# Performance work log

Measured on AMD Instinct MI355X. Metric: run time of the kernel, lower is better.

The kernel has to match this reference:

```python
import jax, jax.numpy as jnp
import numpy as np

IN_F = 128
OUT_F = 64
HEAD = 4
ALPHA = 0.1
N, S = 32, 1024
OH = OUT_F * HEAD


def setup_inputs() -> dict:
    key = jax.random.key(0)
    k_h, k_adj, k_W, k_a = jax.random.split(key, 4)
    h = jax.random.normal(k_h, (N, S, IN_F), dtype=jnp.float32)
    adj = jax.random.uniform(k_adj, (N, S, S), dtype=jnp.float32)
    # xavier_uniform with gain=1.414
    gain = 1.414
    lim_W = gain * np.sqrt(6.0 / (IN_F + OH))
    W = jax.random.uniform(k_W, (IN_F, OH), dtype=jnp.float32, minval=-lim_W, maxval=lim_W)
    lim_a = gain * np.sqrt(6.0 / (2 * OH + 1))
    a = jax.random.uniform(k_a, (2 * OH, 1), dtype=jnp.float32, minval=-lim_a, maxval=lim_a)
    return {"h": h, "adj": adj, "W": W, "a": a}


def reference(h, adj, W, a):
    # h: (N, S, F_in); adj unused in original forward
    Wh = jnp.einsum('nsf,fo->nso', h, W)  # (N, S, OH)
    a1 = a[:OH, 0]   # source half of concat weight
    a2 = a[OH:, 0]   # target half
    # concat([Wh_i, Wh_j]) @ a == Wh_i@a1 + Wh_j@a2  (avoids (N,S,S,2*OH) tensor)
    f = Wh @ a1  # (N, S)
    g = Wh @ a2  # (N, S)
    e = f[:, :, None] + g[:, None, :]          # (N, S, S)
    e = jnp.where(e > 0, e, ALPHA * e)          # LeakyReLU
    attention = jax.nn.softmax(e, axis=2)
    out = jnp.einsum('nij,njo->nio', attention, Wh)  # (N, S, OH)
    # split into HEAD chunks of OUT_F, stack, mean over heads
    out = out.reshape(N, S, HEAD, OUT_F).mean(axis=2)
    # ELU
    return jnp.where(out > 0, out, jnp.expm1(out))
```

## Files before the change

### kernel.cpp

```cpp
#include <hip/hip_runtime.h>
#include <math.h>

#define SQ    1024
#define INF   128
#define OUTF  64
#define OHH   256
#define TSTR  66
#define LOG2E 1.44269504088896f

using bf16x8 = __attribute__((ext_vector_type(8))) __bf16;
using f32x4  = __attribute__((ext_vector_type(4))) float;
using u16x8  = __attribute__((ext_vector_type(8))) unsigned short;

#if __has_builtin(__builtin_amdgcn_exp2f)
#define EXP2F(x) __builtin_amdgcn_exp2f(x)
#else
#define EXP2F(x) __expf((x) * 0.6931471805599453f)
#endif

__global__ __launch_bounds__(256) void kA(
    const float* __restrict__ h, const float* __restrict__ W,
    const float* __restrict__ a, float* __restrict__ whm,
    float* __restrict__ fo, float* __restrict__ go)
{
    __shared__ __bf16 wmfH[8192];
    __shared__ __bf16 wmfL[8192];
    __shared__ float  wfl[INF], wgl[INF];
    __shared__ float  al[2 * OHH];

    const int t    = threadIdx.x;
    const int lane = t & 63;
    const int w    = t >> 6;
    const int bx   = blockIdx.x;
    const int R0   = ((bx & 31) << 10) + ((bx >> 5) << 6);

    al[t]       = a[t];
    al[t + 256] = a[t + 256];

    for (int g = t; g < 2048; g += 256) {
        const int k  = g >> 4;
        const int n0 = (g & 15) << 2;
        const float* Wp = W + k * OHH + n0;
        float4 w0 = *(const float4*)Wp;
        float4 w1 = *(const float4*)(Wp + 64);
        float4 w2 = *(const float4*)(Wp + 128);
        float4 w3 = *(const float4*)(Wp + 192);
        float wm4[4] = {0.25f * (w0.x + w1.x + w2.x + w3.x),
                        0.25f * (w0.y + w1.y + w2.y + w3.y),
                        0.25f * (w0.z + w1.z + w2.z + w3.z),
                        0.25f * (w0.w + w1.w + w2.w + w3.w)};
        const int c = k >> 5, kq = (k >> 3) & 3, id8 = k & 7, T = n0 >> 4;
        const int lbase = kq * 16 + (n0 & 15);
        #pragma unroll
        for (int j = 0; j < 4; ++j) {
            float  v  = wm4[j];
            __bf16 hb = (__bf16)v;
            const int o = ((c * 4 + T) * 64 + lbase + j) * 8 + id8;
            wmfH[o] = hb;
            wmfL[o] = (__bf16)(v - (float)hb);
        }
    }
    __syncthreads();

    {
        const int row = t & 127;
        const float4* Wr = (const float4*)(W + row * OHH);
        const float4* av = (const float4*)(t < 128 ? al : al + OHH);
        float s = 0.f;
        for (int q = 0; q < OHH / 4; ++q) {
            float4 wv = Wr[q], x = av[q];
            s += wv.x * x.x + wv.y * x.y + wv.z * x.z + wv.w * x.w;
        }
        if (t < 128) wfl[row] = s * LOG2E;
        else         wgl[row] = s * LOG2E;
    }
    __syncthreads();

    const int m  = lane & 15;
    const int kq = lane >> 4;
    const float* hrow = h + (size_t)(R0 + w * 16 + m) * INF + kq * 8;

    f32x4 acc[4] = {};
    float sf = 0.f, sg = 0.f;

    #pragma unroll
    for (int c = 0; c < 4; ++c) {
        float4 v0 = *(const float4*)(hrow + c * 32);
        float4 v1 = *(const float4*)(hrow + c * 32 + 4);
        float hv[8] = {v0.x, v0.y, v0.z, v0.w, v1.x, v1.y, v1.z, v1.w};

        float4 wf0 = *(const float4*)(wfl + c * 32 + kq * 8);
        float4 wf1 = *(const float4*)(wfl + c * 32 + kq * 8 + 4);
        float4 wg0 = *(const float4*)(wgl + c * 32 + kq * 8);
        float4 wg1 = *(const float4*)(wgl + c * 32 + kq * 8 + 4);
        float wfv[8] = {wf0.x, wf0.y, wf0.z, wf0.w, wf1.x, wf1.y, wf1.z, wf1.w};
        float wgv[8] = {wg0.x, wg0.y, wg0.z, wg0.w, wg1.x, wg1.y, wg1.z, wg1.w};

        u16x8  ahu;
        bf16x8 alo;
        #pragma unroll
        for (int i = 0; i < 8; ++i) {
            float v = hv[i];
            sf = fmaf(v, wfv[i], sf);
            sg = fmaf(v, wgv[i], sg);
            unsigned u = __float_as_uint(v);
            ahu[i] = (unsigned short)(u >> 16);
            alo[i] = (__bf16)(v - __uint_as_float(u & 0xFFFF0000u));
        }
        bf16x8 ah = __builtin_bit_cast(bf16x8, ahu);

        #pragma unroll
        for (int T = 0; T < 4; ++T) {
            bf16x8 bh = *(const bf16x8*)&wmfH[((c * 4 + T) * 64 + lane) * 8];
            bf16x8 bl = *(const bf16x8*)&wmfL[((c * 4 + T) * 64 + lane) * 8];
            acc[T] = __builtin_amdgcn_mfma_f32_16x16x32_bf16(ah,  bh, acc[T], 0, 0, 0);
            acc[T] = __builtin_amdgcn_mfma_f32_16x16x32_bf16(alo, bh, acc[T], 0, 0, 0);
            acc[T] = __builtin_amdgcn_mfma_f32_16x16x32_bf16(ah,  bl, acc[T], 0, 0, 0);
        }
    }

    sf += __shfl_xor(sf, 16, 64); sf += __shfl_xor(sf, 32, 64);
    sg += __shfl_xor(sg, 16, 64); sg += __shfl_xor(sg, 32, 64);
    if (lane < 16) {
        fo[R0 + w * 16 + m] = sf;
        go[R0 + w * 16 + m] = sg;
    }

    #pragma unroll
    for (int T = 0; T < 4; ++T) {
        #pragma unroll
        for (int r = 0; r < 4; ++r) {
            whm[(size_t)(R0 + w * 16 + kq * 4 + r) * OUTF + T * 16 + m] = acc[T][r];
        }
    }
}

__global__ __launch_bounds__(256) void kR(
    const float* __restrict__ gi, float* __restrict__ gs_out,
    unsigned short* __restrict__ piG)
{
    __shared__ unsigned long long keys[1024];

    const int t  = threadIdx.x;
    const int n  = blockIdx.x & 31;
    const int qb = blockIdx.x >> 5;

    for (int i = t; i < 1024; i += 256) {
        unsigned u   = __float_as_uint(gi[n * SQ + i]);
        unsigned key = (u & 0x80000000u) ? ~u : (u | 0x80000000u);
        keys[i] = ((unsigned long long)key << 32) | (unsigned)i;
    }
    __syncthreads();

    const int el = t >> 2;
    const int qt = t & 3;
    const int e  = qb * 64 + el;
    const unsigned long long Ke = keys[e];

    int cnt = 0;
    #pragma unroll 16
    for (int s = 0; s < 256; ++s) {
        int idx = qt * 256 + ((s + qt * 4) & 255);
        cnt += (keys[idx] < Ke) ? 1 : 0;
    }
    cnt += __shfl_xor(cnt, 1, 64);
    cnt += __shfl_xor(cnt, 2, 64);

    if (qt == 0) {
        unsigned kk = (unsigned)(Ke >> 32);
        unsigned uu = (kk & 0x80000000u) ? (kk & 0x7fffffffu) : ~kk;
        gs_out[n * SQ + cnt] = __uint_as_float(uu);
        piG[n * SQ + cnt]    = (unsigned short)e;
    }
}

__global__ __launch_bounds__(256) void kTB3(
    const float* __restrict__ whm, const unsigned short* __restrict__ piG,
    const float* __restrict__ gs,
    float* __restrict__ sufA, float* __restrict__ preB)
{
    __shared__ float          wsel[1024];
    __shared__ unsigned short piL[1024];
    __shared__ float          tot[16][TSTR];

    const int t    = threadIdx.x;
    const int lane = t & 63;
    const int wid  = t >> 6;
    const int n    = blockIdx.x & 31;
    const int k    = blockIdx.x >> 5;
    const int dir  = k & 1;
    const int qu   = k >> 1;

    for (int i = t; i < 1024; i += 256) {
        float g = gs[n * SQ + i];
        wsel[i] = EXP2F(dir ? g : 0.1f * g);
        piL[i]  = piG[n * SQ + i];
    }
    __syncthreads();

    const float* wb = whm + (size_t)n * (SQ * OUTF);

    for (int cc = 0; cc < 4; ++cc) {
        const int c = wid * 4 + cc;
        float acc = 0.f, dacc = 0.f;
        for (int q0 = 0; q0 < 64; q0 += 16) {
            float vals[16], wvv[16];
            #pragma unroll
            for (int u = 0; u < 16; ++u) {
                int tt = c * 64 + q0 + u;
                wvv[u]  = wsel[tt];
                vals[u] = wb[(size_t)piL[tt] * OUTF + lane];
            }
            #pragma unroll
            for (int u = 0; u < 16; ++u) {
                acc  = fmaf(wvv[u], vals[u], acc);
                dacc += wvv[u];
            }
        }
        tot[c][lane] = acc;
        if (lane == 0) tot[c][64] = dacc;
    }
    __syncthreads();

    const int c = qu * 4 + wid;
    float base = 0.f, based = 0.f;
    if (dir == 0) {
        for (int cc2 = 0; cc2 < c; ++cc2) {
            base  += tot[cc2][lane];
            based += tot[cc2][64];
        }
        float* Gp = preB + ((size_t)n * 1025 + (size_t)c * 64) * TSTR;
        float acc = base, dacc = based;
        for (int q0 = 0; q0 < 64; q0 += 16) {
            float vals[16], wvv[16];
            #pragma unroll
            for (int u = 0; u < 16; ++u) {
                int tt = c * 64 + q0 + u;
                wvv[u]  = wsel[tt];
                vals[u] = wb[(size_t)piL[tt] * OUTF + lane];
            }
            #pragma unroll
            for (int u = 0; u < 16; ++u) {
                float* row = Gp + (size_t)(q0 + u) * TSTR;
                row[lane] = acc;
                if (lane == 0) row[64] = dacc;
                acc  = fmaf(wvv[u], vals[u], acc);
                dacc += wvv[u];
            }
        }
        if (c == 15) {
            float* row = preB + ((size_t)n * 1025 + 1024) * TSTR;
            row[lane] = acc;
            if (lane == 0) row[64] = dacc;
        }
    } else {
        for (int cc2 = c + 1; cc2 < 16; ++cc2) {
            base  += tot[cc2][lane];
            based += tot[cc2][64];
        }
        float* Gs = sufA + ((size_t)n * 1025 + (size_t)c * 64) * TSTR;
        float acc = base, dacc = based;
        for (int q0 = 48; q0 >= 0; q0 -= 16) {
            float vals[16], wvv[16];
            #pragma unroll
            for (int u = 0; u < 16; ++u) {
                int tt = c * 64 + q0 + u;
                wvv[u]  = wsel[tt];
                vals[u] = wb[(size_t)piL[tt] * OUTF + lane];
            }
            #pragma unroll
            for (int u = 15; u >= 0; --u) {
                acc  = fmaf(wvv[u], vals[u], acc);
                dacc += wvv[u];
                float* row = Gs + (size_t)(q0 + u) * TSTR;
                row[lane] = acc;
                if (lane == 0) row[64] = dacc;
            }
        }
        if (c == 15) {
            float* row = sufA + ((size_t)n * 1025 + 1024) * TSTR;
            row[lane] = 0.f;
            if (lane == 0) row[64] = 0.f;
        }
    }
}

__global__ __launch_bounds__(256) void kD(
    const float* __restrict__ fi, const float* __restrict__ gs,
    const float* __restrict__ sufA, const float* __restrict__ preB,
    float* __restrict__ out)
{
    __shared__ float gsL[1025];

    const int t    = threadIdx.x;
    const int lane = t & 63;
    const int wid  = t >> 6;
    const int n    = blockIdx.x & 31;
    const int i0   = (blockIdx.x >> 5) * 64;

    for (int q = t; q < 1024; q += 256) gsL[q] = gs[n * SQ + q];
    if (t == 0) gsL[1024] = 3.0e38f;
    __syncthreads();

    const float myf = fi[n * SQ + i0 + wid * 16 + (lane & 15)];
    const float v = -myf;
    int lo = 0, hi = 1024;
    #pragma unroll
    for (int it = 0; it < 10; ++it) {
        int mid = (lo + hi) >> 1;
        bool gt = gsL[mid] > v;
        hi = gt ? mid : hi;
        lo = gt ? lo : mid + 1;
    }

    const float* SA = sufA + (size_t)n * 1025 * TSTR;
    const float* PB = preB + (size_t)n * 1025 * TSTR;
    const size_t orow0 = (size_t)(n * SQ + i0 + wid * 16);

    #pragma unroll 4
    for (int s = 0; s < 16; ++s) {
        int   r  = __shfl(lo,  s, 64);
        float fv = __shfl(myf, s, 64);
        const float* sa = SA + (size_t)r * TSTR;
        const float* pb = PB + (size_t)r * TSTR;
        float sv = sa[lane], pv = pb[lane];
        float sd = sa[64],  pd = pb[64];
        float eP = EXP2F(fv);
        float eN = EXP2F(0.1f * fv);
        float num = eP * sv + eN * pv;
        float den = eP * sd + eN * pd;
        float o = num / den;
        o = o > 0.f ? o : expm1f(o);
        out[(orow0 + s) * OUTF + lane] = o;
    }
}

extern "C" void kernel_launch(void* const* d_in, const int* in_sizes, int n_in,
                              void* d_out, int out_size, void* d_ws, size_t ws_size,
                              hipStream_t stream) {
    const float* h = (const float*)d_in[0];
    const float* W = (const float*)d_in[2];
    const float* a = (const float*)d_in[3];

    char* ws = (char*)d_ws;
    const size_t MB = 1024 * 1024;
    const size_t KB = 1024;
    float*          whm  = (float*)(ws);
    float*          fb   = (float*)(ws + 8 * MB);
    float*          gb   = (float*)(ws + 8 * MB + 128 * KB);
    float*          gsO  = (float*)(ws + 8 * MB + 256 * KB);
    unsigned short* piG  = (unsigned short*)(ws + 8 * MB + 384 * KB);
    float*          sufA = (float*)(ws + 10 * MB);
    float*          preB = (float*)(ws + 19 * MB);
    float*          outp = (float*)d_out;

    hipLaunchKernelGGL(kA,   dim3(512), dim3(256), 0, stream, h, W, a, whm, fb, gb);
    hipLaunchKernelGGL(kR,   dim3(512), dim3(256), 0, stream, gb, gsO, piG);
    hipLaunchKernelGGL(kTB3, dim3(256), dim3(256), 0, stream, whm, piG, gsO, sufA, preB);
    hipLaunchKernelGGL(kD,   dim3(512), dim3(256), 0, stream, fb, gsO, sufA, preB, outp);
}
```

Before: 227.6 us.

## Split prefix-scan into 32-row chunks, double kTB3 grid, reuse gathered rows

The prefix/suffix scan kernel now splits each batch's 1024 sorted rows into 32 chunks of 32 instead of 16 chunks of 64, and launches twice as many blocks. Each wave keeps the gathered values and weights for its own chunk in registers during the chunk-total pass, so the second gather from global memory is skipped. The kD output loop is also fully unrolled. In exchange, every block still recomputes the totals for all chunks, so redundant gather work doubles across the larger grid, and the 64 kept registers per thread raise register pressure.

```diff
diff --git a/kernel.cpp b/kernel.cpp
--- a/kernel.cpp
+++ b/kernel.cpp
@@ -181,7 +181,7 @@
 {
     __shared__ float          wsel[1024];
     __shared__ unsigned short piL[1024];
-    __shared__ float          tot[16][TSTR];
+    __shared__ float          tot[32][TSTR];
 
     const int t    = threadIdx.x;
     const int lane = t & 63;
@@ -189,7 +189,7 @@
     const int n    = blockIdx.x & 31;
     const int k    = blockIdx.x >> 5;
     const int dir  = k & 1;
-    const int qu   = k >> 1;
+    const int grp  = k >> 1;
 
     for (int i = t; i < 1024; i += 256) {
         float g = gs[n * SQ + i];
@@ -200,14 +200,16 @@
 
     const float* wb = whm + (size_t)n * (SQ * OUTF);
 
-    for (int cc = 0; cc < 4; ++cc) {
-        const int c = wid * 4 + cc;
+    float keepV[32], keepW[32];
+    for (int s8 = 0; s8 < 8; ++s8) {
+        const int sc = s8 * 4 + wid;
         float acc = 0.f, dacc = 0.f;
-        for (int q0 = 0; q0 < 64; q0 += 16) {
+        #pragma unroll
+        for (int h16 = 0; h16 < 2; ++h16) {
             float vals[16], wvv[16];
             #pragma unroll
             for (int u = 0; u < 16; ++u) {
-                int tt = c * 64 + q0 + u;
+                int tt = sc * 32 + h16 * 16 + u;
                 wvv[u]  = wsel[tt];
                 vals[u] = wb[(size_t)piL[tt] * OUTF + lane];
             }
@@ -216,68 +218,57 @@
                 acc  = fmaf(wvv[u], vals[u], acc);
                 dacc += wvv[u];
             }
-        }
-        tot[c][lane] = acc;
-        if (lane == 0) tot[c][64] = dacc;
-    }
-    __syncthreads();
-
-    const int c = qu * 4 + wid;
+            if (s8 == grp) {
+                #pragma unroll
+                for (int u = 0; u < 16; ++u) {
+                    keepV[h16 * 16 + u] = vals[u];
+                    keepW[h16 * 16 + u] = wvv[u];
+                }
+            }
+        }
+        tot[sc][lane] = acc;
+        if (lane == 0) tot[sc][64] = dacc;
+    }
+    __syncthreads();
+
+    const int sc = grp * 4 + wid;
     float base = 0.f, based = 0.f;
     if (dir == 0) {
-        for (int cc2 = 0; cc2 < c; ++cc2) {
-            base  += tot[cc2][lane];
-            based += tot[cc2][64];
-        }
-        float* Gp = preB + ((size_t)n * 1025 + (size_t)c * 64) * TSTR;
+        for (int s = 0; s < sc; ++s) {
+            base  += tot[s][lane];
+            based += tot[s][64];
+        }
+        float* Gp = preB + ((size_t)n * 1025 + (size_t)sc * 32) * TSTR;
         float acc = base, dacc = based;
-        for (int q0 = 0; q0 < 64; q0 += 16) {
-            float vals[16], wvv[16];
-            #pragma unroll
-            for (int u = 0; u < 16; ++u) {
-                int tt = c * 64 + q0 + u;
-                wvv[u]  = wsel[tt];
-                vals[u] = wb[(size_t)piL[tt] * OUTF + lane];
-            }
-            #pragma unroll
-            for (int u = 0; u < 16; ++u) {
-                float* row = Gp + (size_t)(q0 + u) * TSTR;
-                row[lane] = acc;
-                if (lane == 0) row[64] = dacc;
-                acc  = fmaf(wvv[u], vals[u], acc);
-                dacc += wvv[u];
-            }
-        }
-        if (c == 15) {
+        #pragma unroll
+        for (int u = 0; u < 32; ++u) {
+            float* row = Gp + (size_t)u * TSTR;
+            row[lane] = acc;
+            if (lane == 0) row[64] = dacc;
+            acc  = fmaf(keepW[u], keepV[u], acc);
+            dacc += keepW[u];
+        }
+        if (sc == 31) {
             float* row = preB + ((size_t)n * 1025 + 1024) * TSTR;
             row[lane] = acc;
             if (lane == 0) row[64] = dacc;
         }
     } else {
-        for (int cc2 = c + 1; cc2 < 16; ++cc2) {
-            base  += tot[cc2][lane];
-            based += tot[cc2][64];
-        }
-        float* Gs = sufA + ((size_t)n * 1025 + (size_t)c * 64) * TSTR;
+        for (int s = sc + 1; s < 32; ++s) {
+            base  += tot[s][lane];
+            based += tot[s][64];
+        }
+        float* Gs = sufA + ((size_t)n * 1025 + (size_t)sc * 32) * TSTR;
         float acc = base, dacc = based;
-        for (int q0 = 48; q0 >= 0; q0 -= 16) {
-            float vals[16], wvv[16];
-            #pragma unroll
-            for (int u = 0; u < 16; ++u) {
-                int tt = c * 64 + q0 + u;
-                wvv[u]  = wsel[tt];
-                vals[u] = wb[(size_t)piL[tt] * OUTF + lane];
-            }
-            #pragma unroll
-            for (int u = 15; u >= 0; --u) {
-                acc  = fmaf(wvv[u], vals[u], acc);
-                dacc += wvv[u];
-                float* row = Gs + (size_t)(q0 + u) * TSTR;
-                row[lane] = acc;
-                if (lane == 0) row[64] = dacc;
-            }
-        }
-        if (c == 15) {
+        #pragma unroll
+        for (int u = 31; u >= 0; --u) {
+            acc  = fmaf(keepW[u], keepV[u], acc);
+            dacc += keepW[u];
+            float* row = Gs + (size_t)u * TSTR;
+            row[lane] = acc;
+            if (lane == 0) row[64] = dacc;
+        }
+        if (sc == 31) {
             float* row = sufA + ((size_t)n * 1025 + 1024) * TSTR;
             row[lane] = 0.f;
             if (lane == 0) row[64] = 0.f;
@@ -317,7 +308,7 @@
     const float* PB = preB + (size_t)n * 1025 * TSTR;
     const size_t orow0 = (size_t)(n * SQ + i0 + wid * 16);
 
-    #pragma unroll 4
+    #pragma unroll
     for (int s = 0; s < 16; ++s) {
         int   r  = __shfl(lo,  s, 64);
         float fv = __shfl(myf, s, 64);
@@ -356,6 +347,6 @@
 
     hipLaunchKernelGGL(kA,   dim3(512), dim3(256), 0, stream, h, W, a, whm, fb, gb);
     hipLaunchKernelGGL(kR,   dim3(512), dim3(256), 0, stream, gb, gsO, piG);
-    hipLaunchKernelGGL(kTB3, dim3(256), dim3(256), 0, stream, whm, piG, gsO, sufA, preB);
+    hipLaunchKernelGGL(kTB3, dim3(512), dim3(256), 0, stream, whm, piG, gsO, sufA, preB);
     hipLaunchKernelGGL(kD,   dim3(512), dim3(256), 0, stream, fb, gsO, sufA, preB, outp);
 }
```

New measurement: 230.8 us. Within noise of the previous version (+1.4%).
